# Kernel optimization log

Hardware: AMD Instinct MI355X
Metric: run time of the kernel (lower is better)

## Reference

```python
import jax, jax.numpy as jnp
import numpy as np
from jax import lax

THRESH = 0.5
DECAY = 0.2
LENS = 0.5

@jax.custom_vjp
def act_fun(x):
    return (x > THRESH).astype(x.dtype)

def _act_fwd(x):
    return act_fun(x), x

def _act_bwd(x, g):
    return (g * (jnp.abs(x - THRESH) < LENS).astype(g.dtype),)

act_fun.defvjp(_act_fwd, _act_bwd)

def conv2d(x, w, b, stride):
    y = lax.conv_general_dilated(x, w, (stride, stride), 'VALID',
                                 dimension_numbers=('NCHW', 'OIHW', 'NCHW'))
    return y + b[None, :, None, None]

def setup_inputs() -> dict:
    key = jax.random.key(0)
    ks = jax.random.split(key, 7)
    B = 32
    std = float(np.sqrt(3.0 / (8 * 16)))
    data = jax.random.uniform(ks[0], (B, 1, 28, 28), dtype=jnp.float32)
    conv_w = jax.random.normal(ks[1], (256, 1, 9, 9), dtype=jnp.float32) * float(np.sqrt(1.0 / 81))
    conv_b = jax.random.normal(ks[2], (256,), dtype=jnp.float32) * 0.01
    prim_w = jax.random.normal(ks[3], (256, 256, 9, 9), dtype=jnp.float32) * float(np.sqrt(1.0 / (256 * 81)))
    prim_b = jax.random.normal(ks[4], (256,), dtype=jnp.float32) * 0.01
    W = jax.random.normal(ks[5], (1152, 10, 16, 8), dtype=jnp.float32) * std
    bias = jax.random.normal(ks[6], (16, 1), dtype=jnp.float32) * std
    return {"data": data, "conv_w": conv_w, "conv_b": conv_b,
            "prim_w": prim_w, "prim_b": prim_b, "W": W, "bias": bias,
            "time_window": 5}

def capsnet_forward(data, conv_w, conv_b, prim_w, prim_b, W, bias, time_window):
    B = data.shape[0]
    R, C, O = 1152, 10, 16  # num_routes, num_capsules, out_channels
    f32 = jnp.float32
    conv_mem = conv_spike = jnp.zeros((B, 256, 20, 20), f32)
    prim_mem = prim_spike = jnp.zeros((B, R, 8), f32)
    dig_mem = dig_spike = jnp.zeros((B, R, C, O), f32)
    dig2_mem = dig2_spike = jnp.zeros((B, C, O), f32)
    out_mem = jnp.zeros((B, C, O), f32)
    trace_u = jnp.zeros((B, R, C, O), f32)
    b_ij = jnp.ones((1, R, C), f32) / R  # [1,1152,10] (trailing 1 dim dropped)
    decay_tr = jnp.exp(jnp.asarray(-1.0 / 1.5, f32))

    for _ in range(time_window):
        # conv layer membrane update
        conv_out = jax.nn.relu(conv2d(data, conv_w, conv_b, 1))  # [B,256,20,20]
        conv_mem = (conv_mem - conv_spike * THRESH) * DECAY + conv_out
        conv_spike = act_fun(conv_mem)
        # primary caps: 8 parallel convs fused into one (out chans 8*32), then view [B,1152,8]
        prim_out = conv2d(conv_spike, prim_w, prim_b, 2).reshape(B, R, 8)
        prim_mem = (prim_mem - prim_spike * THRESH) * DECAY + prim_out
        prim_spike = act_fun(prim_mem)
        # digit caps: u_hat = W @ x + bias  -> [B,R,C,O]
        u_hat = jnp.einsum('rcoi,bri->brco', W, prim_spike) + bias[:, 0]
        dig_mem = (dig_mem - dig_spike * THRESH) * DECAY + u_hat
        dig_spike = act_fun(dig_mem)
        # digit caps 2: routing-weighted sum over routes
        s_j = jnp.einsum('rc,brco->bco', b_ij[0], dig_spike)  # [B,C,O]
        dig2_mem = (dig2_mem - dig2_spike * THRESH) * DECAY + s_j
        dig2_spike = act_fun(dig2_mem)
        out_mem = out_mem + s_j
        # training-time b_ij / trace update (no_grad in torch)
        ds = lax.stop_gradient(dig_spike)
        d2s = lax.stop_gradient(dig2_spike)
        b_ij = jnp.clip(b_ij, -0.05, 1.0)
        trace_u = jnp.where(ds != 0, 1.0, trace_u * decay_tr)
        delta = 0.0008 * jnp.einsum('brco,bco->brc', trace_u - 0.1, d2s).mean(axis=0)
        b_ij = lax.stop_gradient(b_ij + delta[None])

    output = out_mem / time_window          # [B,10,16]
    classes = jnp.sqrt((output ** 2).sum(2))  # Decoder -> [B,10]
    return classes

def reference(data, conv_w, conv_b, prim_w, prim_b, W, bias, time_window):
    return capsnet_forward(data, conv_w, conv_b, prim_w, prim_b, W, bias, time_window)
```

## Files before the change

kernel.cpp:

```cpp
#include <hip/hip_runtime.h>
#include <stdint.h>

#define THRESH 0.5f
#define DECAY  0.2f
#define TSTEPS 5

#define B_        32
#define CONV_ELEMS (32*256*20*20)
#define RR        1152
#define CC        10
#define PRIM_ELEMS (32*1152*8)
#define DIG_ELEMS  (32*1152*160)
#define MM        256
#define NN        1152
#define KK        20736
#define KSPLIT    18
#define NCH64     18
#define NGG       324

typedef __attribute__((ext_vector_type(4))) int   int32x4;
typedef __attribute__((ext_vector_type(4))) float f32x4;

__device__ __forceinline__ void async16(void* l, const void* g) {
    __builtin_amdgcn_global_load_lds(
        (const __attribute__((address_space(1))) uint32_t*)g,
        (__attribute__((address_space(3))) uint32_t*)l, 16, 0, 0);
}

__global__ void k_init_bij(float* bij) {
    int i = blockIdx.x * 256 + threadIdx.x;
    if (i < RR * CC) bij[i] = 1.0f / 1152.0f;
}

__global__ __launch_bounds__(256) void k_absmax(const float* __restrict__ w,
                                                unsigned* __restrict__ out) {
    __shared__ float sm[4];
    const f32x4* w4 = (const f32x4*)w;
    float m = 0.f;
    for (int i = blockIdx.x * 256 + threadIdx.x; i < MM * KK / 4; i += 256 * 256) {
        f32x4 v = w4[i];
        m = fmaxf(m, fmaxf(fmaxf(fabsf(v.x), fabsf(v.y)),
                           fmaxf(fabsf(v.z), fabsf(v.w))));
    }
    #pragma unroll
    for (int off = 1; off < 64; off <<= 1)
        m = fmaxf(m, __shfl_xor(m, off));
    int lane = threadIdx.x & 63, wv = threadIdx.x >> 6;
    if (lane == 0) sm[wv] = m;
    __syncthreads();
    if (threadIdx.x == 0) {
        float r = fmaxf(fmaxf(sm[0], sm[1]), fmaxf(sm[2], sm[3]));
        atomicMax(out, __float_as_uint(r));
    }
}

__global__ __launch_bounds__(320) void k_conv1(const float* __restrict__ data,
                                               const float* __restrict__ cw,
                                               const float* __restrict__ cb,
                                               float* __restrict__ out) {
    __shared__ float sdat[784];
    __shared__ float swt[1296];
    __shared__ float sout[20 * 333];
    int b = blockIdx.x, og = blockIdx.y;
    int tid = threadIdx.x;
    for (int i = tid; i < 196; i += 320)
        ((f32x4*)sdat)[i] = ((const f32x4*)(data + b * 784))[i];
    for (int i = tid; i < 324; i += 320)
        ((f32x4*)swt)[i] = ((const f32x4*)(cw + og * 1296))[i];
    __syncthreads();
    int ocl = tid / 20, y = tid % 20;
    float acc[20];
    #pragma unroll
    for (int x = 0; x < 20; ++x) acc[x] = 0.f;
    const float* wb = &swt[ocl * 81];
    #pragma unroll
    for (int ky = 0; ky < 9; ++ky) {
        const float* dr = &sdat[(y + ky) * 28];
        float d[28];
        #pragma unroll
        for (int t4 = 0; t4 < 7; ++t4) {
            f32x4 v = ((const f32x4*)dr)[t4];
            d[t4 * 4 + 0] = v.x; d[t4 * 4 + 1] = v.y;
            d[t4 * 4 + 2] = v.z; d[t4 * 4 + 3] = v.w;
        }
        float w[9];
        #pragma unroll
        for (int q = 0; q < 9; ++q) w[q] = wb[ky * 9 + q];
        #pragma unroll
        for (int kx = 0; kx < 9; ++kx)
            #pragma unroll
            for (int x = 0; x < 20; ++x)
                acc[x] += d[x + kx] * w[kx];
    }
    float bias = cb[og * 16 + ocl];
    #pragma unroll
    for (int x = 0; x < 20; ++x)
        sout[y * 333 + x * 16 + ocl] = fmaxf(acc[x] + bias, 0.f);
    __syncthreads();
    const size_t base = (size_t)b * 102400 + og * 16;
    for (int f = tid; f < 6400; f += 320) {
        int yy = f / 320, rem = f % 320;
        out[base + (size_t)(f >> 4) * 256 + (f & 15)] = sout[yy * 333 + rem];
    }
}

__global__ __launch_bounds__(256) void k_wsplit(const float* __restrict__ w,
                                                signed char* __restrict__ A2,
                                                const unsigned* __restrict__ mb) {
    int t = blockIdx.x * 256 + threadIdx.x;
    if (t >= 16 * NGG * 64) return;
    float inv = 32512.f / fmaxf(__uint_as_float(mb[0]), 1e-30f);
    int lane = t & 63;
    int rest = t >> 6;
    int gg = rest % NGG;
    int rowblk = rest / NGG;
    int row = rowblk * 16 + (lane & 15);
    int k0 = gg * 64 + (lane >> 4) * 16;
    union { signed char b[16]; int32x4 v; } H, L;
    #pragma unroll
    for (int j = 0; j < 16; ++j) {
        int k = k0 + j;
        int kw = k >> 8, ic = k & 255;
        float f = w[((size_t)row * 256 + ic) * 81 + kw];
        int q = (int)lrintf(f * inv);
        int lo = (int)(signed char)(q & 0xFF);
        int hi = (q - lo) >> 8;
        H.b[j] = (signed char)hi;
        L.b[j] = (signed char)lo;
    }
    size_t base = ((size_t)(rowblk * NGG + gg) * 2) * 1024 + lane * 16;
    *(int32x4*)(A2 + base)        = H.v;
    *(int32x4*)(A2 + base + 1024) = L.v;
}

__global__ void k_convall(const float* __restrict__ cout, unsigned char* __restrict__ spk5) {
    int i = blockIdx.x * 256 + threadIdx.x;
    if (i >= CONV_ELEMS / 4) return;
    f32x4 c = ((const f32x4*)cout)[i];
    f32x4 m = {0.f, 0.f, 0.f, 0.f};
    #pragma unroll
    for (int t = 0; t < TSTEPS; ++t) {
        unsigned pv = 0;
        #pragma unroll
        for (int j = 0; j < 4; ++j) {
            float mv = m[j];
            float ps = (mv > THRESH) ? THRESH : 0.f;
            mv = (mv - ps) * DECAY + c[j];
            m[j] = mv;
            if (mv > THRESH) pv |= (1u << (8 * j));
        }
        ((unsigned*)(spk5 + (size_t)t * CONV_ELEMS))[i] = pv;
    }
}

__device__ __forceinline__ void bij_body(int g, const uint8_t* __restrict__ age,
                                         const float* __restrict__ d2mem,
                                         float* __restrict__ bij) {
    int r = g / 160, co = g % 160, c = co / 16, o = co & 15;
    const float dtr = expf(-1.0f / 1.5f);
    float tab[5];
    tab[0] = 1.f;
    #pragma unroll
    for (int k = 1; k < 5; ++k) tab[k] = tab[k - 1] * dtr;
    float acc = 0.f;
    #pragma unroll 8
    for (int b = 0; b < B_; ++b) {
        uint8_t a = age[(size_t)b * (RR * 160) + g];
        float tv = (a == 0 || a > 5) ? 0.f : tab[a - 1];
        float d2 = (d2mem[b * 160 + co] > THRESH) ? 1.f : 0.f;
        acc += (tv - 0.1f) * d2;
    }
    #pragma unroll
    for (int off = 1; off < 16; off <<= 1) acc += __shfl_xor(acc, off);
    if (o == 0) {
        float bo = bij[r * 10 + c];
        bo = fminf(fmaxf(bo, -0.05f), 1.0f);
        bij[r * 10 + c] = bo + 0.0008f * (acc * (1.0f / 32.0f));
    }
}

__global__ __launch_bounds__(256) void k_gemm(const signed char* __restrict__ A2,
                                              const unsigned char* __restrict__ spk,
                                              int* __restrict__ Ci,
                                              int do_bij,
                                              const uint8_t* __restrict__ age,
                                              const float* __restrict__ d2mem,
                                              float* __restrict__ bij) {
    __shared__ signed char sB[3][128 * 64];
    int bid = blockIdx.x;
    int tid = threadIdx.x;
    if (bid >= 648) {
        if (!do_bij) return;
        int g = (bid - 648) * 256 + tid;
        bij_body(g, age, d2mem, bij);
        return;
    }
    int slot = bid & 7, j = bid >> 3;
    int tm = slot & 3, kpar = slot >> 2;
    int tn = j / 9, ks2 = j % 9;
    int ks = ks2 * 2 + kpar;

    int rbB[2], slB[2];
    #pragma unroll
    for (int p = 0; p < 2; ++p) {
        int f = p * 256 + tid;
        int n = f >> 2;
        slB[p] = (f & 3) ^ (n & 3) ^ ((n >> 2) & 3);
        int gn = tn * 128 + n;
        int b = gn / 36, pos = gn % 36;
        rbB[p] = ((b * 20 + (pos / 6) * 2) * 20 + (pos % 6) * 2) * 256;
    }

    int wid = tid >> 6, lane = tid & 63;
    int wr = wid >> 1, wc = wid & 1;
    int fr = lane & 15, sl = lane >> 4;

    const signed char* pA[2][2];
    #pragma unroll
    for (int d = 0; d < 2; ++d)
        #pragma unroll
        for (int i = 0; i < 2; ++i) {
            int blk = tm * 4 + wr * 2 + i;
            pA[d][i] = A2 + ((size_t)((blk * NGG + ks * NCH64) * 2 + d)) * 1024 + lane * 16;
        }

    int offB[4];
    #pragma unroll
    for (int jj = 0; jj < 4; ++jj) {
        int n = wc * 64 + jj * 16 + fr;
        offB[jj] = n * 64 + ((sl ^ (n & 3) ^ ((n >> 2) & 3)) << 4);
    }

#define STAGE(buf, c) do {                                                       \
        _Pragma("unroll")                                                        \
        for (int p = 0; p < 2; ++p) {                                            \
            int kp_ = ks * 1152 + (c) * 64 + slB[p] * 16;                        \
            int kw_ = kp_ >> 8, ic_ = kp_ & 255;                                 \
            async16(&sB[buf][(p * 256 + tid) * 16],                              \
                    spk + rbB[p] + ((kw_ / 9) * 20 + (kw_ % 9)) * 256 + ic_);    \
        }                                                                        \
    } while (0)

#define LOADA(dst, c) do {                                                       \
        _Pragma("unroll")                                                        \
        for (int d = 0; d < 2; ++d)                                              \
            _Pragma("unroll")                                                    \
            for (int i = 0; i < 2; ++i)                                          \
                dst[d][i] = *(const int32x4*)(pA[d][i] + (size_t)(c) * 2048);    \
    } while (0)

#define ITER(c, CUR, NXT) do {                                                   \
        asm volatile("s_waitcnt vmcnt(6)" ::: "memory");                         \
        __builtin_amdgcn_s_barrier();                                            \
        if ((c) + 2 < NCH64) STAGE(((c) + 2) % 3, (c) + 2);                      \
        if ((c) + 1 < NCH64) LOADA(NXT, (c) + 1);                                \
        int32x4 bv[4];                                                           \
        const signed char* sbc = sB[(c) % 3];                                    \
        _Pragma("unroll")                                                        \
        for (int jj = 0; jj < 4; ++jj) bv[jj] = *(const int32x4*)&sbc[offB[jj]]; \
        _Pragma("unroll")                                                        \
        for (int i = 0; i < 2; ++i)                                              \
            _Pragma("unroll")                                                    \
            for (int jj = 0; jj < 4; ++jj) {                                     \
                accH[i][jj] = __builtin_amdgcn_mfma_i32_16x16x64_i8(             \
                    CUR[0][i], bv[jj], accH[i][jj], 0, 0, 0);                    \
                accL[i][jj] = __builtin_amdgcn_mfma_i32_16x16x64_i8(             \
                    CUR[1][i], bv[jj], accL[i][jj], 0, 0, 0);                    \
            }                                                                    \
    } while (0)

    int32x4 accH[2][4] = {};
    int32x4 accL[2][4] = {};
    int32x4 aA[2][2], aB[2][2];
    STAGE(0, 0);
    STAGE(1, 1);
    LOADA(aA, 0);
    for (int c = 0; c < NCH64; c += 2) {
        ITER(c, aA, aB);
        ITER(c + 1, aB, aA);
    }
#undef ITER
#undef LOADA
#undef STAGE

    int colb = lane & 15, rb4 = (lane >> 4) * 4;
    #pragma unroll
    for (int i = 0; i < 2; ++i)
        #pragma unroll
        for (int jj = 0; jj < 4; ++jj) {
            int gm = tm * 64 + wr * 32 + i * 16 + rb4;
            int gn = tn * 128 + wc * 64 + jj * 16 + colb;
            #pragma unroll
            for (int q = 0; q < 4; ++q)
                atomicAdd(&Ci[(size_t)(gm + q) * NN + gn],
                          accH[i][jj][q] * 256 + accL[i][jj][q]);
        }
}

__global__ __launch_bounds__(320) void k_dig(const int* __restrict__ Ci,
                                             const unsigned* __restrict__ mb,
                                             const float* __restrict__ pb,
                                             float* __restrict__ pmem,
                                             const float* __restrict__ W,
                                             const float* __restrict__ bias,
                                             const float* __restrict__ bij,
                                             float* __restrict__ dmem,
                                             uint8_t* __restrict__ age,
                                             float* __restrict__ sjp) {
    __shared__ float ps[128];
    int r0 = blockIdx.x * 4;
    int by = blockIdx.y;
    int tid = threadIdx.x;
    if (tid < 128) {
        float s1 = fmaxf(__uint_as_float(mb[0]), 1e-30f) / 32512.f;
        int bl = tid >> 5, ff = tid & 31;
        int f = r0 * 8 + ff;
        int oc = f / 36, pos = f % 36;
        int b = by * 4 + bl;
        int n = b * 36 + pos;
        float sacc = pb[oc] + (float)Ci[(size_t)oc * NN + n] * s1;
        size_t pidx = (size_t)b * 9216 + f;
        float m = pmem[pidx];
        float pso = (m > THRESH) ? THRESH : 0.f;
        m = (m - pso) * DECAY + sacc;
        pmem[pidx] = m;
        ps[(ff >> 3) * 32 + bl * 8 + (ff & 7)] = (m > THRESH) ? 1.f : 0.f;
    }
    __syncthreads();
    int co = tid % 160, bh = tid / 160;
    int c = co >> 4, o = co & 15;
    float bo = bias[o];

    size_t idx8[4][2];
    float  m8[4][2];
    uint8_t a8[4][2];
    #pragma unroll
    for (int r = 0; r < 4; ++r)
        #pragma unroll
        for (int bb = 0; bb < 2; ++bb) {
            int bl = bh * 2 + bb;
            idx8[r][bb] = ((size_t)((by * 4 + bl) * 1152 + r0 + r)) * 160 + co;
            m8[r][bb] = dmem[idx8[r][bb]];
            a8[r][bb] = age[idx8[r][bb]];
        }

    float sacc2[2] = {0.f, 0.f};
    #pragma unroll
    for (int r = 0; r < 4; ++r) {
        int rr = r0 + r;
        const float* wp = W + ((size_t)((rr * 10 + c) * 16 + o)) * 8;
        f32x4 w0 = *(const f32x4*)wp;
        f32x4 w1 = *(const f32x4*)(wp + 4);
        float bv = bij[rr * 10 + c];
        #pragma unroll
        for (int bb = 0; bb < 2; ++bb) {
            const float* p8 = &ps[r * 32 + (bh * 2 + bb) * 8];
            f32x4 pa = *(const f32x4*)p8;
            f32x4 pc = *(const f32x4*)(p8 + 4);
            float u = bo + w0.x * pa.x + w0.y * pa.y + w0.z * pa.z + w0.w * pa.w
                         + w1.x * pc.x + w1.y * pc.y + w1.z * pc.z + w1.w * pc.w;
            float m = m8[r][bb];
            float psv = (m > THRESH) ? THRESH : 0.f;
            m = (m - psv) * DECAY + u;
            dmem[idx8[r][bb]] = m;
            bool sp = m > THRESH;
            if (sp) sacc2[bb] += bv;
            uint8_t a = a8[r][bb];
            age[idx8[r][bb]] = sp ? (uint8_t)1 : (a ? (uint8_t)(a + 1) : (uint8_t)0);
        }
    }
    size_t pbase = ((size_t)(by * 288 + blockIdx.x)) * 640;
    #pragma unroll
    for (int bb = 0; bb < 2; ++bb)
        sjp[pbase + (bh * 2 + bb) * 160 + co] = sacc2[bb];
}

__global__ void k_dig2a(const float* __restrict__ sjp, float* __restrict__ sjp2,
                        int* __restrict__ Ci) {
    int bx = blockIdx.x;
    int tid = threadIdx.x;
    if (bx < 240) {
        int gx = bx % 20, ky = bx / 20;
        int e = gx * 256 + tid;
        int b = e / 160, co = e % 160;
        int y = b >> 2, rem = (b & 3) * 160 + co;
        int x0 = ky * 24;
        float a = 0.f;
        #pragma unroll 8
        for (int x = x0; x < x0 + 24; ++x)
            a += sjp[((size_t)(y * 288 + x)) * 640 + rem];
        sjp2[ky * 5120 + e] = a;
    } else {
        int idx = (bx - 240) * 256 + tid;
        int32x4 z = {0, 0, 0, 0};
        ((int32x4*)Ci)[idx] = z;
    }
}

__global__ void k_dig2b(const float* __restrict__ sjp2, float* __restrict__ d2mem,
                        float* __restrict__ omem) {
    int e = blockIdx.x * 256 + threadIdx.x;
    if (e >= B_ * 160) return;
    float s = 0.f;
    #pragma unroll
    for (int k = 0; k < 12; ++k) s += sjp2[k * 5120 + e];
    float m = d2mem[e];
    float ps = (m > THRESH) ? THRESH : 0.f;
    d2mem[e] = (m - ps) * DECAY + s;
    omem[e] += s;
}

__global__ void k_out(const float* __restrict__ omem, float* __restrict__ out) {
    int i = blockIdx.x * 64 + threadIdx.x;
    if (i >= B_ * CC) return;
    int b = i / 10, c = i % 10;
    float s = 0.f;
    #pragma unroll
    for (int o = 0; o < 16; ++o) {
        float v = omem[b * 160 + c * 16 + o] / 5.0f;
        s += v * v;
    }
    out[i] = sqrtf(s);
}

extern "C" void kernel_launch(void* const* d_in, const int* in_sizes, int n_in,
                              void* d_out, int out_size, void* d_ws, size_t ws_size,
                              hipStream_t stream) {
    const float* data   = (const float*)d_in[0];
    const float* conv_w = (const float*)d_in[1];
    const float* conv_b = (const float*)d_in[2];
    const float* prim_w = (const float*)d_in[3];
    const float* prim_b = (const float*)d_in[4];
    const float* W      = (const float*)d_in[5];
    const float* bias   = (const float*)d_in[6];
    float* out = (float*)d_out;

    char* ws = (char*)d_ws;
    size_t off = 0;
    auto alloc = [&](size_t bytes) {
        void* p = ws + off;
        off = (off + bytes + 255) & ~(size_t)255;
        return p;
    };
    size_t zbase = off;
    float*          prim_mem = (float*)alloc((size_t)PRIM_ELEMS * 4);
    float*          dig_mem  = (float*)alloc((size_t)DIG_ELEMS * 4);
    float*          dig2_mem = (float*)alloc(5120 * 4);
    float*          out_mem  = (float*)alloc(5120 * 4);
    uint8_t*        age      = (uint8_t*)alloc(DIG_ELEMS);
    unsigned*       mb       = (unsigned*)alloc(256);
    int*            Ci       = (int*)alloc((size_t)MM * NN * 4);
    size_t zbytes = off - zbase;
    float*          conv_out = (float*)alloc((size_t)CONV_ELEMS * 4);
    unsigned char*  spk5     = (unsigned char*)alloc((size_t)TSTEPS * CONV_ELEMS);
    float*          sjp      = (float*)alloc((size_t)2304 * 640 * 4);
    float*          sjp2     = (float*)alloc((size_t)12 * 5120 * 4);
    float*          bij      = (float*)alloc(RR * CC * 4);
    signed char*    A2       = (signed char*)alloc((size_t)MM * KK * 2);

    hipMemsetAsync(ws + zbase, 0, zbytes, stream);

    k_init_bij<<<(RR * CC + 255) / 256, 256, 0, stream>>>(bij);
    k_absmax<<<256, 256, 0, stream>>>(prim_w, mb);
    k_conv1<<<dim3(32, 16), 320, 0, stream>>>(data, conv_w, conv_b, conv_out);
    k_wsplit<<<(16 * NGG * 64 + 255) / 256, 256, 0, stream>>>(prim_w, A2, mb);
    k_convall<<<(CONV_ELEMS / 4 + 255) / 256, 256, 0, stream>>>(conv_out, spk5);

    for (int t = 0; t < TSTEPS; ++t) {
        int do_bij = (t > 0);
        int ggrid = 648 + (do_bij ? 720 : 0);
        k_gemm<<<ggrid, 256, 0, stream>>>(A2, spk5 + (size_t)t * CONV_ELEMS, Ci,
                                          do_bij, age, dig2_mem, bij);
        k_dig<<<dim3(288, 8), 320, 0, stream>>>(Ci, mb, prim_b, prim_mem, W, bias,
                                                bij, dig_mem, age, sjp);
        k_dig2a<<<528, 256, 0, stream>>>(sjp, sjp2, Ci);
        k_dig2b<<<20, 256, 0, stream>>>(sjp2, dig2_mem, out_mem);
    }
    k_out<<<(B_ * CC + 63) / 64, 64, 0, stream>>>(out_mem, out);
}
```

Before: 367.5 us.

## Load GEMM B operand directly from global instead of LDS triple-buffering

The int8 GEMM kernel stops staging spike tiles into a triple-buffered LDS ring with async global-to-LDS copies and barriers. Each wave now reads its B fragments straight from global memory (relying on cache) alongside the A fragments, with the loop unrolled by 3. This removes LDS usage, barriers and the swizzle bookkeeping, which may raise occupancy. In exchange it loses explicit prefetch overlap and duplicates B reads across the waves that share columns.

```diff
diff --git a/kernel.cpp b/kernel.cpp
--- a/kernel.cpp
+++ b/kernel.cpp
@@ -20,12 +20,6 @@
 
 typedef __attribute__((ext_vector_type(4))) int   int32x4;
 typedef __attribute__((ext_vector_type(4))) float f32x4;
-
-__device__ __forceinline__ void async16(void* l, const void* g) {
-    __builtin_amdgcn_global_load_lds(
-        (const __attribute__((address_space(1))) uint32_t*)g,
-        (__attribute__((address_space(3))) uint32_t*)l, 16, 0, 0);
-}
 
 __global__ void k_init_bij(float* bij) {
     int i = blockIdx.x * 256 + threadIdx.x;
@@ -186,7 +180,6 @@
                                               const uint8_t* __restrict__ age,
                                               const float* __restrict__ d2mem,
                                               float* __restrict__ bij) {
-    __shared__ signed char sB[3][128 * 64];
     int bid = blockIdx.x;
     int tid = threadIdx.x;
     if (bid >= 648) {
@@ -200,21 +193,18 @@
     int tn = j / 9, ks2 = j % 9;
     int ks = ks2 * 2 + kpar;
 
-    int rbB[2], slB[2];
-    #pragma unroll
-    for (int p = 0; p < 2; ++p) {
-        int f = p * 256 + tid;
-        int n = f >> 2;
-        slB[p] = (f & 3) ^ (n & 3) ^ ((n >> 2) & 3);
-        int gn = tn * 128 + n;
-        int b = gn / 36, pos = gn % 36;
-        rbB[p] = ((b * 20 + (pos / 6) * 2) * 20 + (pos % 6) * 2) * 256;
-    }
-
     int wid = tid >> 6, lane = tid & 63;
     int wr = wid >> 1, wc = wid & 1;
     int fr = lane & 15, sl = lane >> 4;
 
+    const unsigned char* pB[4];
+    #pragma unroll
+    for (int jj = 0; jj < 4; ++jj) {
+        int gn = tn * 128 + wc * 64 + jj * 16 + fr;
+        int b = gn / 36, pos = gn % 36;
+        pB[jj] = spk + ((b * 20 + (pos / 6) * 2) * 20 + (pos % 6) * 2) * 256;
+    }
+
     const signed char* pA[2][2];
     #pragma unroll
     for (int d = 0; d < 2; ++d)
@@ -224,64 +214,33 @@
             pA[d][i] = A2 + ((size_t)((blk * NGG + ks * NCH64) * 2 + d)) * 1024 + lane * 16;
         }
 
-    int offB[4];
-    #pragma unroll
-    for (int jj = 0; jj < 4; ++jj) {
-        int n = wc * 64 + jj * 16 + fr;
-        offB[jj] = n * 64 + ((sl ^ (n & 3) ^ ((n >> 2) & 3)) << 4);
-    }
-
-#define STAGE(buf, c) do {                                                       \
-        _Pragma("unroll")                                                        \
-        for (int p = 0; p < 2; ++p) {                                            \
-            int kp_ = ks * 1152 + (c) * 64 + slB[p] * 16;                        \
-            int kw_ = kp_ >> 8, ic_ = kp_ & 255;                                 \
-            async16(&sB[buf][(p * 256 + tid) * 16],                              \
-                    spk + rbB[p] + ((kw_ / 9) * 20 + (kw_ % 9)) * 256 + ic_);    \
-        }                                                                        \
-    } while (0)
-
-#define LOADA(dst, c) do {                                                       \
-        _Pragma("unroll")                                                        \
-        for (int d = 0; d < 2; ++d)                                              \
-            _Pragma("unroll")                                                    \
-            for (int i = 0; i < 2; ++i)                                          \
-                dst[d][i] = *(const int32x4*)(pA[d][i] + (size_t)(c) * 2048);    \
-    } while (0)
-
-#define ITER(c, CUR, NXT) do {                                                   \
-        asm volatile("s_waitcnt vmcnt(6)" ::: "memory");                         \
-        __builtin_amdgcn_s_barrier();                                            \
-        if ((c) + 2 < NCH64) STAGE(((c) + 2) % 3, (c) + 2);                      \
-        if ((c) + 1 < NCH64) LOADA(NXT, (c) + 1);                                \
-        int32x4 bv[4];                                                           \
-        const signed char* sbc = sB[(c) % 3];                                    \
-        _Pragma("unroll")                                                        \
-        for (int jj = 0; jj < 4; ++jj) bv[jj] = *(const int32x4*)&sbc[offB[jj]]; \
-        _Pragma("unroll")                                                        \
-        for (int i = 0; i < 2; ++i)                                              \
-            _Pragma("unroll")                                                    \
-            for (int jj = 0; jj < 4; ++jj) {                                     \
-                accH[i][jj] = __builtin_amdgcn_mfma_i32_16x16x64_i8(             \
-                    CUR[0][i], bv[jj], accH[i][jj], 0, 0, 0);                    \
-                accL[i][jj] = __builtin_amdgcn_mfma_i32_16x16x64_i8(             \
-                    CUR[1][i], bv[jj], accL[i][jj], 0, 0, 0);                    \
-            }                                                                    \
-    } while (0)
-
     int32x4 accH[2][4] = {};
     int32x4 accL[2][4] = {};
-    int32x4 aA[2][2], aB[2][2];
-    STAGE(0, 0);
-    STAGE(1, 1);
-    LOADA(aA, 0);
-    for (int c = 0; c < NCH64; c += 2) {
-        ITER(c, aA, aB);
-        ITER(c + 1, aB, aA);
-    }
-#undef ITER
-#undef LOADA
-#undef STAGE
+    #pragma unroll 3
+    for (int c = 0; c < NCH64; ++c) {
+        int kp = ks * 1152 + c * 64 + sl * 16;
+        int kw = kp >> 8, ic = kp & 255;
+        int koff = ((kw / 9) * 20 + (kw % 9)) * 256 + ic;
+        int32x4 bv[4];
+        #pragma unroll
+        for (int jj = 0; jj < 4; ++jj)
+            bv[jj] = *(const int32x4*)(pB[jj] + koff);
+        int32x4 av[2][2];
+        #pragma unroll
+        for (int d = 0; d < 2; ++d)
+            #pragma unroll
+            for (int i = 0; i < 2; ++i)
+                av[d][i] = *(const int32x4*)(pA[d][i] + (size_t)c * 2048);
+        #pragma unroll
+        for (int i = 0; i < 2; ++i)
+            #pragma unroll
+            for (int jj = 0; jj < 4; ++jj) {
+                accH[i][jj] = __builtin_amdgcn_mfma_i32_16x16x64_i8(
+                    av[0][i], bv[jj], accH[i][jj], 0, 0, 0);
+                accL[i][jj] = __builtin_amdgcn_mfma_i32_16x16x64_i8(
+                    av[1][i], bv[jj], accL[i][jj], 0, 0, 0);
+            }
+    }
 
     int colb = lane & 15, rb4 = (lane >> 4) * 4;
     #pragma unroll
```

After: 385.7 us. +4.9%, slower.

## Batch all timestep GEMMs into one launch with split-K partials and reduction

Applied to the files above, without the earlier changes.

The conv spike trains for all five timesteps are known up front, so the primary-caps GEMM now runs once over all timesteps in a single 1620-block launch. It uses a 9-way K split with 36 chunks each, writing partial sums to a buffer instead of doing atomicAdds. A separate k_cred kernel sums the partials per timestep, and the b_ij update moves to its own kernel at the end of each loop iteration. This removes the per-step atomics, the Ci zeroing and the serialized GEMM launches, but adds about 47 MB of partial-sum traffic and an extra reduction pass.

```diff
diff --git a/kernel.cpp b/kernel.cpp
--- a/kernel.cpp
+++ b/kernel.cpp
@@ -14,8 +14,8 @@
 #define MM        256
 #define NN        1152
 #define KK        20736
-#define KSPLIT    18
-#define NCH64     18
+#define KSPLIT    9
+#define NCH64     36
 #define NGG       324
 
 typedef __attribute__((ext_vector_type(4))) int   int32x4;
@@ -153,52 +153,18 @@
     }
 }
 
-__device__ __forceinline__ void bij_body(int g, const uint8_t* __restrict__ age,
-                                         const float* __restrict__ d2mem,
-                                         float* __restrict__ bij) {
-    int r = g / 160, co = g % 160, c = co / 16, o = co & 15;
-    const float dtr = expf(-1.0f / 1.5f);
-    float tab[5];
-    tab[0] = 1.f;
-    #pragma unroll
-    for (int k = 1; k < 5; ++k) tab[k] = tab[k - 1] * dtr;
-    float acc = 0.f;
-    #pragma unroll 8
-    for (int b = 0; b < B_; ++b) {
-        uint8_t a = age[(size_t)b * (RR * 160) + g];
-        float tv = (a == 0 || a > 5) ? 0.f : tab[a - 1];
-        float d2 = (d2mem[b * 160 + co] > THRESH) ? 1.f : 0.f;
-        acc += (tv - 0.1f) * d2;
-    }
-    #pragma unroll
-    for (int off = 1; off < 16; off <<= 1) acc += __shfl_xor(acc, off);
-    if (o == 0) {
-        float bo = bij[r * 10 + c];
-        bo = fminf(fmaxf(bo, -0.05f), 1.0f);
-        bij[r * 10 + c] = bo + 0.0008f * (acc * (1.0f / 32.0f));
-    }
-}
-
 __global__ __launch_bounds__(256) void k_gemm(const signed char* __restrict__ A2,
-                                              const unsigned char* __restrict__ spk,
-                                              int* __restrict__ Ci,
-                                              int do_bij,
-                                              const uint8_t* __restrict__ age,
-                                              const float* __restrict__ d2mem,
-                                              float* __restrict__ bij) {
+                                              const unsigned char* __restrict__ spk5,
+                                              int* __restrict__ Cp5) {
     __shared__ signed char sB[3][128 * 64];
     int bid = blockIdx.x;
     int tid = threadIdx.x;
-    if (bid >= 648) {
-        if (!do_bij) return;
-        int g = (bid - 648) * 256 + tid;
-        bij_body(g, age, d2mem, bij);
-        return;
-    }
-    int slot = bid & 7, j = bid >> 3;
-    int tm = slot & 3, kpar = slot >> 2;
-    int tn = j / 9, ks2 = j % 9;
-    int ks = ks2 * 2 + kpar;
+    int t = bid / 324;
+    int r = bid % 324;
+    int tm = r & 3;
+    int j = r >> 2;
+    int tn = j / 9, ks = j % 9;
+    const unsigned char* spk = spk5 + (size_t)t * CONV_ELEMS;
 
     int rbB[2], slB[2];
     #pragma unroll
@@ -234,7 +200,7 @@
 #define STAGE(buf, c) do {                                                       \
         _Pragma("unroll")                                                        \
         for (int p = 0; p < 2; ++p) {                                            \
-            int kp_ = ks * 1152 + (c) * 64 + slB[p] * 16;                        \
+            int kp_ = ks * 2304 + (c) * 64 + slB[p] * 16;                        \
             int kw_ = kp_ >> 8, ic_ = kp_ & 255;                                 \
             async16(&sB[buf][(p * 256 + tid) * 16],                              \
                     spk + rbB[p] + ((kw_ / 9) * 20 + (kw_ % 9)) * 256 + ic_);    \
@@ -284,6 +250,7 @@
 #undef STAGE
 
     int colb = lane & 15, rb4 = (lane >> 4) * 4;
+    int* Co = Cp5 + (size_t)(t * KSPLIT + ks) * (MM * NN);
     #pragma unroll
     for (int i = 0; i < 2; ++i)
         #pragma unroll
@@ -292,9 +259,49 @@
             int gn = tn * 128 + wc * 64 + jj * 16 + colb;
             #pragma unroll
             for (int q = 0; q < 4; ++q)
-                atomicAdd(&Ci[(size_t)(gm + q) * NN + gn],
-                          accH[i][jj][q] * 256 + accL[i][jj][q]);
-        }
+                Co[(size_t)(gm + q) * NN + gn] = accH[i][jj][q] * 256 + accL[i][jj][q];
+        }
+}
+
+__global__ __launch_bounds__(256) void k_cred(const int* __restrict__ Cp5,
+                                              int* __restrict__ Ci5) {
+    int i = blockIdx.x * 256 + threadIdx.x;
+    int t = i / 73728, rem = i % 73728;
+    const int32x4* src = (const int32x4*)(Cp5 + (size_t)t * KSPLIT * (MM * NN));
+    int32x4 s = {0, 0, 0, 0};
+    #pragma unroll
+    for (int ks = 0; ks < KSPLIT; ++ks) {
+        int32x4 v = src[(size_t)ks * 73728 + rem];
+        s.x += v.x; s.y += v.y; s.z += v.z; s.w += v.w;
+    }
+    ((int32x4*)(Ci5 + (size_t)t * (MM * NN)))[rem] = s;
+}
+
+__global__ void k_bij(const uint8_t* __restrict__ age, const float* __restrict__ d2mem,
+                      float* __restrict__ bij) {
+    int g = blockIdx.x * 256 + threadIdx.x;
+    if (g >= RR * 160) return;
+    int r = g / 160, co = g % 160, c = co / 16, o = co & 15;
+    const float dtr = expf(-1.0f / 1.5f);
+    float tab[5];
+    tab[0] = 1.f;
+    #pragma unroll
+    for (int k = 1; k < 5; ++k) tab[k] = tab[k - 1] * dtr;
+    float acc = 0.f;
+    #pragma unroll 8
+    for (int b = 0; b < B_; ++b) {
+        uint8_t a = age[(size_t)b * (RR * 160) + g];
+        float tv = (a == 0 || a > 5) ? 0.f : tab[a - 1];
+        float d2 = (d2mem[b * 160 + co] > THRESH) ? 1.f : 0.f;
+        acc += (tv - 0.1f) * d2;
+    }
+    #pragma unroll
+    for (int off = 1; off < 16; off <<= 1) acc += __shfl_xor(acc, off);
+    if (o == 0) {
+        float bo = bij[r * 10 + c];
+        bo = fminf(fmaxf(bo, -0.05f), 1.0f);
+        bij[r * 10 + c] = bo + 0.0008f * (acc * (1.0f / 32.0f));
+    }
 }
 
 __global__ __launch_bounds__(320) void k_dig(const int* __restrict__ Ci,
@@ -375,26 +382,19 @@
         sjp[pbase + (bh * 2 + bb) * 160 + co] = sacc2[bb];
 }
 
-__global__ void k_dig2a(const float* __restrict__ sjp, float* __restrict__ sjp2,
-                        int* __restrict__ Ci) {
+__global__ void k_dig2a(const float* __restrict__ sjp, float* __restrict__ sjp2) {
     int bx = blockIdx.x;
     int tid = threadIdx.x;
-    if (bx < 240) {
-        int gx = bx % 20, ky = bx / 20;
-        int e = gx * 256 + tid;
-        int b = e / 160, co = e % 160;
-        int y = b >> 2, rem = (b & 3) * 160 + co;
-        int x0 = ky * 24;
-        float a = 0.f;
-        #pragma unroll 8
-        for (int x = x0; x < x0 + 24; ++x)
-            a += sjp[((size_t)(y * 288 + x)) * 640 + rem];
-        sjp2[ky * 5120 + e] = a;
-    } else {
-        int idx = (bx - 240) * 256 + tid;
-        int32x4 z = {0, 0, 0, 0};
-        ((int32x4*)Ci)[idx] = z;
-    }
+    int gx = bx % 20, ky = bx / 20;
+    int e = gx * 256 + tid;
+    int b = e / 160, co = e % 160;
+    int y = b >> 2, rem = (b & 3) * 160 + co;
+    int x0 = ky * 24;
+    float a = 0.f;
+    #pragma unroll 8
+    for (int x = x0; x < x0 + 24; ++x)
+        a += sjp[((size_t)(y * 288 + x)) * 640 + rem];
+    sjp2[ky * 5120 + e] = a;
 }
 
 __global__ void k_dig2b(const float* __restrict__ sjp2, float* __restrict__ d2mem,
@@ -449,7 +449,6 @@
     float*          out_mem  = (float*)alloc(5120 * 4);
     uint8_t*        age      = (uint8_t*)alloc(DIG_ELEMS);
     unsigned*       mb       = (unsigned*)alloc(256);
-    int*            Ci       = (int*)alloc((size_t)MM * NN * 4);
     size_t zbytes = off - zbase;
     float*          conv_out = (float*)alloc((size_t)CONV_ELEMS * 4);
     unsigned char*  spk5     = (unsigned char*)alloc((size_t)TSTEPS * CONV_ELEMS);
@@ -457,6 +456,8 @@
     float*          sjp2     = (float*)alloc((size_t)12 * 5120 * 4);
     float*          bij      = (float*)alloc(RR * CC * 4);
     signed char*    A2       = (signed char*)alloc((size_t)MM * KK * 2);
+    int*            Cp5      = (int*)alloc((size_t)TSTEPS * KSPLIT * MM * NN * 4);
+    int*            Ci5      = (int*)alloc((size_t)TSTEPS * MM * NN * 4);
 
     hipMemsetAsync(ws + zbase, 0, zbytes, stream);
 
@@ -466,15 +467,17 @@
     k_wsplit<<<(16 * NGG * 64 + 255) / 256, 256, 0, stream>>>(prim_w, A2, mb);
     k_convall<<<(CONV_ELEMS / 4 + 255) / 256, 256, 0, stream>>>(conv_out, spk5);
 
+    k_gemm<<<TSTEPS * 324, 256, 0, stream>>>(A2, spk5, Cp5);
+    k_cred<<<TSTEPS * 288, 256, 0, stream>>>(Cp5, Ci5);
+
     for (int t = 0; t < TSTEPS; ++t) {
-        int do_bij = (t > 0);
-        int ggrid = 648 + (do_bij ? 720 : 0);
-        k_gemm<<<ggrid, 256, 0, stream>>>(A2, spk5 + (size_t)t * CONV_ELEMS, Ci,
-                                          do_bij, age, dig2_mem, bij);
-        k_dig<<<dim3(288, 8), 320, 0, stream>>>(Ci, mb, prim_b, prim_mem, W, bias,
+        k_dig<<<dim3(288, 8), 320, 0, stream>>>(Ci5 + (size_t)t * (MM * NN), mb,
+                                                prim_b, prim_mem, W, bias,
                                                 bij, dig_mem, age, sjp);
-        k_dig2a<<<528, 256, 0, stream>>>(sjp, sjp2, Ci);
+        k_dig2a<<<240, 256, 0, stream>>>(sjp, sjp2);
         k_dig2b<<<20, 256, 0, stream>>>(sjp2, dig2_mem, out_mem);
+        if (t < TSTEPS - 1)
+            k_bij<<<720, 256, 0, stream>>>(age, dig2_mem, bij);
     }
     k_out<<<(B_ * CC + 63) / 64, 64, 0, stream>>>(out_mem, out);
 }
```

Measured after the change: 307.4 us. -16.4%, faster.
